# Optimization experiments

Measured on AMD Instinct MI355X. Metric: run time of the kernel, lower is better.

Reference implementation:

```python
import jax, jax.numpy as jnp
import numpy as np

E = 64      # embedding_dim
H = 64      # h_dim
MLP = 1024  # mlp_dim (attention hidden)
PRE1 = 512  # mlp_pre_pool hidden
BNK = 1024  # bottleneck_dim
S = 256     # num scenes (equal-size groups replacing seq_start_end)
P = 16      # pedestrians per scene
B = S * P   # total batch of pedestrians
T = 8       # obs_len for vx/vy (only last row used)
EPS = 1e-5  # BatchNorm eps


def _bn(x, g, b, m, v):
    # eval-mode BatchNorm1d over the last (feature) axis
    return (x - m) * jax.lax.rsqrt(v + EPS) * g + b


def setup_inputs() -> dict:
    key = jax.random.key(0)
    ks = jax.random.split(key, 24)
    def n(k, shape, s=1.0):
        return jax.random.normal(k, shape, jnp.float32) * s
    return {
        "h_states": n(ks[0], (1, B, H)),
        "end_pos": n(ks[1], (B, 2)),
        "vx": n(ks[2], (T, B)),
        "vy": n(ks[3], (T, B)),
        "W_sp": n(ks[4], (2, E), 0.05), "b_sp": jnp.zeros((E,), jnp.float32),
        "W_vel": n(ks[5], (2, E), 0.05), "b_vel": jnp.zeros((E,), jnp.float32),
        "Wa1": n(ks[6], (2 * E, MLP), 0.05), "ba1": jnp.zeros((MLP,), jnp.float32),
        "ga1": jnp.ones((MLP,), jnp.float32), "bta1": jnp.zeros((MLP,), jnp.float32),
        "ma1": n(ks[7], (MLP,), 0.1), "va1": jax.random.uniform(ks[8], (MLP,), jnp.float32) + 0.5,
        "Wa2": n(ks[9], (MLP, 1), 0.05), "ba2": jnp.zeros((1,), jnp.float32),
        "ga2": jnp.ones((1,), jnp.float32), "bta2": jnp.zeros((1,), jnp.float32),
        "ma2": n(ks[10], (1,), 0.1), "va2": jax.random.uniform(ks[11], (1,), jnp.float32) + 0.5,
        "Wp1": n(ks[12], (E + H, PRE1), 0.05), "bp1": jnp.zeros((PRE1,), jnp.float32),
        "gp1": jnp.ones((PRE1,), jnp.float32), "btp1": jnp.zeros((PRE1,), jnp.float32),
        "mp1": n(ks[13], (PRE1,), 0.1), "vp1": jax.random.uniform(ks[14], (PRE1,), jnp.float32) + 0.5,
        "Wp2": n(ks[15], (PRE1, BNK), 0.05), "bp2": jnp.zeros((BNK,), jnp.float32),
        "gp2": jnp.ones((BNK,), jnp.float32), "btp2": jnp.zeros((BNK,), jnp.float32),
        "mp2": n(ks[16], (BNK,), 0.1), "vp2": jax.random.uniform(ks[17], (BNK,), jnp.float32) + 0.5,
        "num_scenes": S, "num_ped": P,
    }


def _forward(h_states, end_pos, vx, vy, W_sp, b_sp, W_vel, b_vel,
             Wa1, ba1, ga1, bta1, ma1, va1, Wa2, ba2, ga2, bta2, ma2, va2,
             Wp1, bp1, gp1, btp1, mp1, vp1, Wp2, bp2, gp2, btp2, mp2, vp2,
             num_scenes, num_ped):
    Sn, Pn = num_scenes, num_ped
    h = h_states.reshape(-1, H).reshape(Sn, Pn, H)          # per-scene hidden
    pos = end_pos.reshape(Sn, Pn, 2)
    # rel[s,i,j] = pos[s,j] - pos[s,i]  (repeat vs repeat_interleave in torch)
    rel = pos[:, None, :, :] - pos[:, :, None, :]
    rel_emb = rel @ W_sp + b_sp                              # [S,P,P,E]
    vel = jnp.stack([vx[-1], vy[-1]], axis=-1).reshape(Sn, Pn, 2)
    vel_emb = vel @ W_vel + b_vel                            # [S,P,E], indexed by row i
    vel_emb = jnp.broadcast_to(vel_emb[:, :, None, :], (Sn, Pn, Pn, E))
    att_in = jnp.concatenate([rel_emb, vel_emb], axis=-1)    # [S,P,P,2E]
    a = jax.nn.relu(_bn(att_in @ Wa1 + ba1, ga1, bta1, ma1, va1))
    scores = jax.nn.relu(_bn(a @ Wa2 + ba2, ga2, bta2, ma2, va2))  # [S,P,P,1]
    # torch.softmax(scores, dim=1) on an (N,1) tensor: softmax over the size-1
    # feature axis -> identically 1.0. Reproduced faithfully here.
    w = jax.nn.softmax(scores, axis=-1)
    h_rep = jnp.broadcast_to(h[:, None, :, :], (Sn, Pn, Pn, H))   # h[s,j] per (i,j)
    x = jnp.concatenate([rel_emb, h_rep], axis=-1) * (0.05 * w)   # [S,P,P,E+H]
    y = jax.nn.relu(_bn(x @ Wp1 + bp1, gp1, btp1, mp1, vp1))
    y = jax.nn.relu(_bn(y @ Wp2 + bp2, gp2, btp2, mp2, vp2))      # [S,P,P,BNK]
    pool = jnp.max(y, axis=2)                                     # max over neighbors j
    return pool.reshape(Sn * Pn, BNK)


def reference(h_states, end_pos, vx, vy, W_sp, b_sp, W_vel, b_vel,
              Wa1, ba1, ga1, bta1, ma1, va1, Wa2, ba2, ga2, bta2, ma2, va2,
              Wp1, bp1, gp1, btp1, mp1, vp1, Wp2, bp2, gp2, btp2, mp2, vp2,
              num_scenes, num_ped):
    return _forward(h_states, end_pos, vx, vy, W_sp, b_sp, W_vel, b_vel,
                    Wa1, ba1, ga1, bta1, ma1, va1, Wa2, ba2, ga2, bta2, ma2, va2,
                    Wp1, bp1, gp1, btp1, mp1, vp1, Wp2, bp2, gp2, btp2, mp2, vp2,
                    num_scenes, num_ped)
```

## Files before the change

kernel.cpp:

```cpp
#include <hip/hip_runtime.h>
#include <hip/hip_bf16.h>
#include <stdint.h>


typedef __bf16 bf16x8 __attribute__((ext_vector_type(8)));
typedef __bf16 bf16x2 __attribute__((ext_vector_type(2)));
typedef float  f32x4  __attribute__((ext_vector_type(4)));
typedef float  f32x2  __attribute__((ext_vector_type(2)));
typedef float  f32x16 __attribute__((ext_vector_type(16)));

#define BP2_OFF 0u
#define BP1_OFF 1048576u
#define MX_OFF  1114112u
#define MY_OFF  1116160u
#define CB_OFF  1118208u
#define SH_OFF  1120256u
#define A2_OFF  1122304u
#define C2_OFF  1126400u

#define Y1_LDS  0
#define HH_LDS  131072
#define LDS_SZ  147456

__device__ __forceinline__ unsigned short f2bf(float f) {
    union { float f; unsigned u; } c; c.f = f;
    unsigned u = c.u;
    return (unsigned short)((u + 0x7fffu + ((u >> 16) & 1u)) >> 16);
}
__device__ __forceinline__ float bfbits2f(unsigned hi) {
    union { unsigned u; float f; } c; c.u = hi; return c.f;
}
__device__ __forceinline__ unsigned pk_bf16(float a, float b) {
#if __has_builtin(__builtin_amdgcn_cvt_pk_bf16_f32)
    bf16x2 p = __builtin_amdgcn_cvt_pk_bf16_f32(a, b);
    union { bf16x2 v; unsigned u; } c; c.v = p; return c.u;
#else
    return (unsigned)f2bf(a) | ((unsigned)f2bf(b) << 16);
#endif
}
__device__ __forceinline__ int y1off(int r, int c16) {
    return r * 1024 + ((c16 ^ (r & 7)) << 4);
}

__global__ __launch_bounds__(256) void prep_pack_kernel(
    const float* __restrict__ Wsp,  const float* __restrict__ bsp,
    const float* __restrict__ Wp1,  const float* __restrict__ bp1,
    const float* __restrict__ gp1,  const float* __restrict__ btp1,
    const float* __restrict__ mp1,  const float* __restrict__ vp1,
    const float* __restrict__ Wp2,  const float* __restrict__ bp2,
    const float* __restrict__ gp2,  const float* __restrict__ btp2,
    const float* __restrict__ mp2,  const float* __restrict__ vp2,
    unsigned char* __restrict__ ws)
{
    __shared__ float tile[32 * 65];
    const int blk = blockIdx.x, t = threadIdx.x;

    if (blk < 272) {
        const float* src; int ncols, kb, ng;
        if (blk < 256) { kb = blk >> 4; ng = blk & 15; src = Wp2; ncols = 1024; }
        else { int b2 = blk - 256; kb = b2 >> 3; ng = b2 & 7; src = Wp1 + 64 * 512; ncols = 512; }
        const int k0 = kb * 32, n0 = ng * 64;
        #pragma unroll
        for (int it = 0; it < 2; ++it) {
            int c = t + it * 256;
            int r = c >> 4, c4 = c & 15;
            float4 v = *(const float4*)(src + (k0 + r) * ncols + n0 + c4 * 4);
            tile[r * 65 + c4 * 4 + 0] = v.x;
            tile[r * 65 + c4 * 4 + 1] = v.y;
            tile[r * 65 + c4 * 4 + 2] = v.z;
            tile[r * 65 + c4 * 4 + 3] = v.w;
        }
        __syncthreads();
        if (blk < 256) {
            const int l = t & 63, ch = (t >> 6) & 1, kh = t >> 7;
            const int nl = ch * 32 + (l & 31);
            const int kl = kh * 16 + ((l >> 5) & 1) * 8;
            uint4 o;
            o.x = pk_bf16(tile[(kl + 0) * 65 + nl], tile[(kl + 1) * 65 + nl]);
            o.y = pk_bf16(tile[(kl + 2) * 65 + nl], tile[(kl + 3) * 65 + nl]);
            o.z = pk_bf16(tile[(kl + 4) * 65 + nl], tile[(kl + 5) * 65 + nl]);
            o.w = pk_bf16(tile[(kl + 6) * 65 + nl], tile[(kl + 7) * 65 + nl]);
            const int kstep = kb * 2 + kh, ct = ng * 2 + ch;
            ((uint4*)(ws + BP2_OFF))[(kstep * 32 + ct) * 64 + l] = o;
        } else {
            int ntl = t >> 6, l = t & 63;
            int nl = ntl * 16 + (l & 15), kl = (l >> 4) * 8;
            uint4 o;
            o.x = pk_bf16(tile[(kl + 0) * 65 + nl], tile[(kl + 1) * 65 + nl]);
            o.y = pk_bf16(tile[(kl + 2) * 65 + nl], tile[(kl + 3) * 65 + nl]);
            o.z = pk_bf16(tile[(kl + 4) * 65 + nl], tile[(kl + 5) * 65 + nl]);
            o.w = pk_bf16(tile[(kl + 6) * 65 + nl], tile[(kl + 7) * 65 + nl]);
            ((uint4*)(ws + BP1_OFF))[((ng * 4 + ntl) * 2 + kb) * 64 + l] = o;
        }
    } else if (blk < 274) {
        int k = (blk - 272) * 256 + t;
        float a1 = gp1[k] * rsqrtf(vp1[k] + 1e-5f);
        float mx = 0.f, my = 0.f, cb = 0.f;
        for (int e = 0; e < 64; ++e) {
            float wv = Wp1[e * 512 + k];
            mx = fmaf(Wsp[e],      wv, mx);
            my = fmaf(Wsp[64 + e], wv, my);
            cb = fmaf(bsp[e],      wv, cb);
        }
        ((float*)(ws + MX_OFF))[k] = 0.05f * a1 * mx;
        ((float*)(ws + MY_OFF))[k] = 0.05f * a1 * my;
        ((float*)(ws + CB_OFF))[k] = 0.05f * a1 * cb + (bp1[k] - mp1[k]) * a1 + btp1[k];
        ((float*)(ws + SH_OFF))[k] = 0.05f * a1;
    } else {
        int n = (blk - 274) * 256 + t;
        float a = gp2[n] * rsqrtf(vp2[n] + 1e-5f);
        ((float*)(ws + A2_OFF))[n] = a;
        ((float*)(ws + C2_OFF))[n] = btp2[n] + (bp2[n] - mp2[n]) * a;
    }
}

__global__ __launch_bounds__(512, 2) void mm2_kernel(
    const float* __restrict__ hst,
    const float* __restrict__ epos,
    const unsigned char* __restrict__ ws,
    float* __restrict__ out)
{
    __shared__ __align__(16) unsigned char smem[LDS_SZ];

    const int s   = blockIdx.x >> 1;
    const int ih  = blockIdx.x & 1;
    const int tid = threadIdx.x;
    const int w    = tid >> 6;
    const int l    = tid & 63;
    const int quad = l >> 4;
    const int jl   = l & 15;

    {
        union { unsigned u[4]; bf16x8 v; } afh[2];
        #pragma unroll
        for (int kb = 0; kb < 2; ++kb) {
            const float4* hp = (const float4*)(hst + (s * 16 + jl) * 64 + kb * 32 + quad * 8);
            float4 v0 = hp[0], v1 = hp[1];
            afh[kb].u[0] = pk_bf16(v0.x, v0.y);
            afh[kb].u[1] = pk_bf16(v0.z, v0.w);
            afh[kb].u[2] = pk_bf16(v1.x, v1.y);
            afh[kb].u[3] = pk_bf16(v1.z, v1.w);
        }
        const f32x4 fz = {0.f, 0.f, 0.f, 0.f};
        f32x4 acch[4] = {fz, fz, fz, fz};
        #pragma unroll
        for (int kb = 0; kb < 2; ++kb) {
            #pragma unroll
            for (int ct = 0; ct < 4; ++ct) {
                bf16x8 bfr = *(const bf16x8*)(ws + BP1_OFF + ((((w * 4 + ct) * 2 + kb) * 64 + l) << 4));
                acch[ct] = __builtin_amdgcn_mfma_f32_16x16x32_bf16(afh[kb].v, bfr, acch[ct], 0, 0, 0);
            }
        }
        const float* SHg = (const float*)(ws + SH_OFF);
        const float* CBg = (const float*)(ws + CB_OFF);
        #pragma unroll
        for (int ct = 0; ct < 4; ++ct) {
            int col = (w * 4 + ct) * 16 + jl;
            float sh = SHg[col], cb = CBg[col];
            #pragma unroll
            for (int reg = 0; reg < 4; ++reg) {
                int j = quad * 4 + reg;
                float hv = fmaf(acch[ct][reg], sh, cb);
                *(unsigned short*)(smem + HH_LDS + j * 1024 + col * 2) = f2bf(hv);
            }
        }
    }
    __syncthreads();

    {
        const int i2 = tid >> 8;
        const int j  = (tid >> 4) & 15;
        const int kc = tid & 15;
        float rx[4], ry[4];
        float pjx = epos[s * 32 + j * 2], pjy = epos[s * 32 + j * 2 + 1];
        #pragma unroll
        for (int ii = 0; ii < 4; ++ii) {
            int ig_ = ih * 8 + i2 * 4 + ii;
            rx[ii] = pjx - epos[s * 32 + ig_ * 2];
            ry[ii] = pjy - epos[s * 32 + ig_ * 2 + 1];
        }
        const f32x2 zero2 = {0.f, 0.f};
        #pragma unroll
        for (int kk = 0; kk < 4; ++kk) {
            int k = kc * 32 + kk * 8;
            uint4 hh8 = *(const uint4*)(smem + HH_LDS + j * 1024 + k * 2);
            f32x4 mx0 = *(const f32x4*)(ws + MX_OFF + k * 4);
            f32x4 mx1 = *(const f32x4*)(ws + MX_OFF + k * 4 + 16);
            f32x4 my0 = *(const f32x4*)(ws + MY_OFF + k * 4);
            f32x4 my1 = *(const f32x4*)(ws + MY_OFF + k * 4 + 16);
            f32x2 mxp[4] = { {mx0[0],mx0[1]}, {mx0[2],mx0[3]}, {mx1[0],mx1[1]}, {mx1[2],mx1[3]} };
            f32x2 myp[4] = { {my0[0],my0[1]}, {my0[2],my0[3]}, {my1[0],my1[1]}, {my1[2],my1[3]} };
            f32x2 hhp[4];
            hhp[0][0] = bfbits2f(hh8.x << 16); hhp[0][1] = bfbits2f(hh8.x & 0xffff0000u);
            hhp[1][0] = bfbits2f(hh8.y << 16); hhp[1][1] = bfbits2f(hh8.y & 0xffff0000u);
            hhp[2][0] = bfbits2f(hh8.z << 16); hhp[2][1] = bfbits2f(hh8.z & 0xffff0000u);
            hhp[3][0] = bfbits2f(hh8.w << 16); hhp[3][1] = bfbits2f(hh8.w & 0xffff0000u);
            #pragma unroll
            for (int ii = 0; ii < 4; ++ii) {
                f32x2 rx2 = { rx[ii], rx[ii] };
                f32x2 ry2 = { ry[ii], ry[ii] };
                uint4 o;
                unsigned uu[4];
                #pragma unroll
                for (int p = 0; p < 4; ++p) {
                    f32x2 tt = __builtin_elementwise_fma(ry2, myp[p], hhp[p]);
                    tt = __builtin_elementwise_fma(rx2, mxp[p], tt);
                    tt = __builtin_elementwise_max(tt, zero2);
                    uu[p] = pk_bf16(tt[0], tt[1]);
                }
                o.x = uu[0]; o.y = uu[1]; o.z = uu[2]; o.w = uu[3];
                int r = (i2 * 4 + ii) * 16 + j;
                *(uint4*)(smem + Y1_LDS + y1off(r, kc * 4 + kk)) = o;
            }
        }
    }
    __syncthreads();

    {
        const int lane31 = l & 31;
        const int hi = l >> 5;
        const int sr = lane31 & 7;
        const float* A2 = (const float*)(ws + A2_OFF);
        const float* C2 = (const float*)(ws + C2_OFF);

        int av[4];
        #pragma unroll
        for (int rt = 0; rt < 4; ++rt)
            av[rt] = Y1_LDS + (rt * 32 + lane31) * 1024 + ((hi ^ sr) << 4);

        const f32x16 fz16 = {0.f,0.f,0.f,0.f,0.f,0.f,0.f,0.f,
                             0.f,0.f,0.f,0.f,0.f,0.f,0.f,0.f};

        #pragma unroll 1
        for (int chunk = 0; chunk < 2; ++chunk) {
            const int ctbase = w * 4 + chunk * 2;
            const unsigned char* bp = ws + BP2_OFF + (ctbase << 10) + (l << 4);

            f32x16 acc[4][2];
            #pragma unroll
            for (int rt = 0; rt < 4; ++rt) { acc[rt][0] = fz16; acc[rt][1] = fz16; }

            bf16x8 a0[4], a1[4];
            bf16x8 br[4][2];

            auto ldA = [&](bf16x8* dst, int add, int xorv) {
                #pragma unroll
                for (int rt = 0; rt < 4; ++rt)
                    dst[rt] = *(const bf16x8*)(smem + ((av[rt] + add) ^ xorv));
            };
            auto ldB = [&](bf16x8* slot, const unsigned char* base, int off) {
                slot[0] = *(const bf16x8*)(base + off);
                slot[1] = *(const bf16x8*)(base + off + 1024);
            };
            auto mfma8 = [&](const bf16x8* a, const bf16x8* b) {
                __builtin_amdgcn_s_setprio(1);
                #pragma unroll
                for (int c = 0; c < 2; ++c)
                    #pragma unroll
                    for (int rt = 0; rt < 4; ++rt)
                        acc[rt][c] = __builtin_amdgcn_mfma_f32_32x32x16_bf16(
                            a[rt], b[c], acc[rt][c], 0, 0, 0);
                __builtin_amdgcn_s_setprio(0);
            };

            ldB(br[0], bp, 0);
            ldB(br[1], bp, 32768);
            ldB(br[2], bp, 65536);
            ldA(a0, 0, 0);

            #pragma unroll 1
            for (int kq = 0; kq < 7; ++kq) {
                const unsigned char* bq = bp + kq * 131072;
                const int ka = kq * 128;
                ldB(br[3], bq, 98304);
                ldA(a1, ka, 32);
                mfma8(a0, br[0]);
                ldB(br[0], bq, 131072);
                ldA(a0, ka, 64);
                mfma8(a1, br[1]);
                ldB(br[1], bq, 163840);
                ldA(a1, ka, 96);
                mfma8(a0, br[2]);
                ldB(br[2], bq, 196608);
                ldA(a0, ka + 128, 0);
                mfma8(a1, br[3]);
            }
            {
                const unsigned char* bq = bp + 7 * 131072;
                const int ka = 7 * 128;
                ldB(br[3], bq, 98304);
                ldA(a1, ka, 32);
                mfma8(a0, br[0]);
                ldA(a0, ka, 64);
                mfma8(a1, br[1]);
                ldA(a1, ka, 96);
                mfma8(a0, br[2]);
                mfma8(a1, br[3]);
            }

            #pragma unroll
            for (int c = 0; c < 2; ++c) {
                const int col = (ctbase + c) * 32 + lane31;
                const float a2 = A2[col], c2v = C2[col];
                #pragma unroll
                for (int rt = 0; rt < 4; ++rt) {
                    float mv[2];
                    #pragma unroll
                    for (int hg = 0; hg < 2; ++hg) {
                        float v0 = fmaxf(fmaf(acc[rt][c][hg * 8 + 0], a2, c2v), 0.f);
                        float v1 = fmaxf(fmaf(acc[rt][c][hg * 8 + 1], a2, c2v), 0.f);
                        float v2 = fmaxf(fmaf(acc[rt][c][hg * 8 + 2], a2, c2v), 0.f);
                        float v3 = fmaxf(fmaf(acc[rt][c][hg * 8 + 3], a2, c2v), 0.f);
                        float v4 = fmaxf(fmaf(acc[rt][c][hg * 8 + 4], a2, c2v), 0.f);
                        float v5 = fmaxf(fmaf(acc[rt][c][hg * 8 + 5], a2, c2v), 0.f);
                        float v6 = fmaxf(fmaf(acc[rt][c][hg * 8 + 6], a2, c2v), 0.f);
                        float v7 = fmaxf(fmaf(acc[rt][c][hg * 8 + 7], a2, c2v), 0.f);
                        float m = fmaxf(fmaxf(fmaxf(v0, v1), fmaxf(v2, v3)),
                                        fmaxf(fmaxf(v4, v5), fmaxf(v6, v7)));
                        mv[hg] = fmaxf(m, __shfl_xor(m, 32, 64));
                    }
                    const int iloc = rt * 2 + hi;
                    const float vout = hi ? mv[1] : mv[0];
                    const int orow = s * 16 + ih * 8 + iloc;
                    __builtin_nontemporal_store(vout, &out[orow * 1024 + col]);
                }
            }
        }
    }
}

extern "C" void kernel_launch(void* const* d_in, const int* in_sizes, int n_in,
                              void* d_out, int out_size, void* d_ws, size_t ws_size,
                              hipStream_t stream) {
    const float* hst  = (const float*)d_in[0];
    const float* epos = (const float*)d_in[1];
    const float* Wsp  = (const float*)d_in[4];
    const float* bsp  = (const float*)d_in[5];
    const float* Wp1  = (const float*)d_in[20];
    const float* bp1  = (const float*)d_in[21];
    const float* gp1  = (const float*)d_in[22];
    const float* btp1 = (const float*)d_in[23];
    const float* mp1  = (const float*)d_in[24];
    const float* vp1  = (const float*)d_in[25];
    const float* Wp2  = (const float*)d_in[26];
    const float* bp2  = (const float*)d_in[27];
    const float* gp2  = (const float*)d_in[28];
    const float* btp2 = (const float*)d_in[29];
    const float* mp2  = (const float*)d_in[30];
    const float* vp2  = (const float*)d_in[31];
    unsigned char* ws = (unsigned char*)d_ws;
    float* out = (float*)d_out;

    prep_pack_kernel<<<278, 256, 0, stream>>>(Wsp, bsp, Wp1, bp1, gp1, btp1, mp1, vp1,
                                              Wp2, bp2, gp2, btp2, mp2, vp2, ws);
    mm2_kernel<<<512, 512, 0, stream>>>(hst, epos, ws, out);
}
```

Baseline: 192.1 us.

## Software-pipeline across column chunks with explicit waitcnts and split prep reduction

The two column-chunk GEMM loops in mm2_kernel are flattened so that B loads for the second chunk are issued before the first chunk's epilogue, and explicit s_waitcnt with sched barriers replace compiler-inserted waits, keeping more loads in flight. B loads become nontemporal, setprio calls are dropped, and the BN scale/shift loads are hoisted into registers. The prep kernel's per-k reduction over the embedding dimension is split across four thread groups with an LDS reduction over more blocks, and the y1 LDS write pattern is changed to interleave columns. Hand-written waitcnt counts are fragile and could cause races or stalls if they miscount outstanding operations.

```diff
diff --git a/kernel.cpp b/kernel.cpp
--- a/kernel.cpp
+++ b/kernel.cpp
@@ -21,6 +21,9 @@
 #define Y1_LDS  0
 #define HH_LDS  131072
 #define LDS_SZ  147456
+
+#define WAITCNT(S) do { asm volatile("s_waitcnt " S ::: "memory"); \
+                        __builtin_amdgcn_sched_barrier(0); } while (0)
 
 __device__ __forceinline__ unsigned short f2bf(float f) {
     union { float f; unsigned u; } c; c.f = f;
@@ -53,6 +56,7 @@
     unsigned char* __restrict__ ws)
 {
     __shared__ float tile[32 * 65];
+    __shared__ float part[3][4][64];
     const int blk = blockIdx.x, t = threadIdx.x;
 
     if (blk < 272) {
@@ -92,22 +96,33 @@
             o.w = pk_bf16(tile[(kl + 6) * 65 + nl], tile[(kl + 7) * 65 + nl]);
             ((uint4*)(ws + BP1_OFF))[((ng * 4 + ntl) * 2 + kb) * 64 + l] = o;
         }
-    } else if (blk < 274) {
-        int k = (blk - 272) * 256 + t;
-        float a1 = gp1[k] * rsqrtf(vp1[k] + 1e-5f);
+    } else if (blk < 280) {
+        const int kk = t & 63, eq = t >> 6;
+        const int k = (blk - 272) * 64 + kk;
         float mx = 0.f, my = 0.f, cb = 0.f;
-        for (int e = 0; e < 64; ++e) {
+        #pragma unroll
+        for (int e2 = 0; e2 < 16; ++e2) {
+            int e = eq * 16 + e2;
             float wv = Wp1[e * 512 + k];
             mx = fmaf(Wsp[e],      wv, mx);
             my = fmaf(Wsp[64 + e], wv, my);
             cb = fmaf(bsp[e],      wv, cb);
         }
-        ((float*)(ws + MX_OFF))[k] = 0.05f * a1 * mx;
-        ((float*)(ws + MY_OFF))[k] = 0.05f * a1 * my;
-        ((float*)(ws + CB_OFF))[k] = 0.05f * a1 * cb + (bp1[k] - mp1[k]) * a1 + btp1[k];
-        ((float*)(ws + SH_OFF))[k] = 0.05f * a1;
+        part[0][eq][kk] = mx; part[1][eq][kk] = my; part[2][eq][kk] = cb;
+        __syncthreads();
+        if (t < 64) {
+            const int k2 = (blk - 272) * 64 + t;
+            float mxs = part[0][0][t] + part[0][1][t] + part[0][2][t] + part[0][3][t];
+            float mys = part[1][0][t] + part[1][1][t] + part[1][2][t] + part[1][3][t];
+            float cbs = part[2][0][t] + part[2][1][t] + part[2][2][t] + part[2][3][t];
+            float a1 = gp1[k2] * rsqrtf(vp1[k2] + 1e-5f);
+            ((float*)(ws + MX_OFF))[k2] = 0.05f * a1 * mxs;
+            ((float*)(ws + MY_OFF))[k2] = 0.05f * a1 * mys;
+            ((float*)(ws + CB_OFF))[k2] = 0.05f * a1 * cbs + (bp1[k2] - mp1[k2]) * a1 + btp1[k2];
+            ((float*)(ws + SH_OFF))[k2] = 0.05f * a1;
+        }
     } else {
-        int n = (blk - 274) * 256 + t;
+        int n = (blk - 280) * 256 + t;
         float a = gp2[n] * rsqrtf(vp2[n] + 1e-5f);
         ((float*)(ws + A2_OFF))[n] = a;
         ((float*)(ws + C2_OFF))[n] = btp2[n] + (bp2[n] - mp2[n]) * a;
@@ -182,7 +197,8 @@
         const f32x2 zero2 = {0.f, 0.f};
         #pragma unroll
         for (int kk = 0; kk < 4; ++kk) {
-            int k = kc * 32 + kk * 8;
+            int c16 = kk * 16 + kc;
+            int k = c16 * 8;
             uint4 hh8 = *(const uint4*)(smem + HH_LDS + j * 1024 + k * 2);
             f32x4 mx0 = *(const f32x4*)(ws + MX_OFF + k * 4);
             f32x4 mx1 = *(const f32x4*)(ws + MX_OFF + k * 4 + 16);
@@ -210,7 +226,7 @@
                 }
                 o.x = uu[0]; o.y = uu[1]; o.z = uu[2]; o.w = uu[3];
                 int r = (i2 * 4 + ii) * 16 + j;
-                *(uint4*)(smem + Y1_LDS + y1off(r, kc * 4 + kk)) = o;
+                *(uint4*)(smem + Y1_LDS + y1off(r, c16)) = o;
             }
         }
     }
@@ -231,90 +247,49 @@
         const f32x16 fz16 = {0.f,0.f,0.f,0.f,0.f,0.f,0.f,0.f,
                              0.f,0.f,0.f,0.f,0.f,0.f,0.f,0.f};
 
-        #pragma unroll 1
-        for (int chunk = 0; chunk < 2; ++chunk) {
-            const int ctbase = w * 4 + chunk * 2;
-            const unsigned char* bp = ws + BP2_OFF + (ctbase << 10) + (l << 4);
-
-            f32x16 acc[4][2];
-            #pragma unroll
-            for (int rt = 0; rt < 4; ++rt) { acc[rt][0] = fz16; acc[rt][1] = fz16; }
-
-            bf16x8 a0[4], a1[4];
-            bf16x8 br[4][2];
-
-            auto ldA = [&](bf16x8* dst, int add, int xorv) {
+        const int ctb0 = w * 4;
+        const unsigned char* bp = ws + BP2_OFF + (ctb0 << 10) + (l << 4);
+
+        f32x16 acc[4][2];
+        bf16x8 a0[4], a1[4];
+        bf16x8 br[4][2];
+        float a2v[2], c2v[2];
+
+        auto ldA = [&](bf16x8* dst, int add, int xorv) {
+            #pragma unroll
+            for (int rt = 0; rt < 4; ++rt)
+                dst[rt] = *(const bf16x8*)(smem + ((av[rt] + add) ^ xorv));
+        };
+        auto ldB = [&](bf16x8* slot, const unsigned char* p) {
+            slot[0] = __builtin_nontemporal_load((const bf16x8*)p);
+            slot[1] = __builtin_nontemporal_load((const bf16x8*)(p + 1024));
+        };
+        auto mfma8 = [&](const bf16x8* a, const bf16x8* b) {
+            #pragma unroll
+            for (int c = 0; c < 2; ++c)
                 #pragma unroll
                 for (int rt = 0; rt < 4; ++rt)
-                    dst[rt] = *(const bf16x8*)(smem + ((av[rt] + add) ^ xorv));
-            };
-            auto ldB = [&](bf16x8* slot, const unsigned char* base, int off) {
-                slot[0] = *(const bf16x8*)(base + off);
-                slot[1] = *(const bf16x8*)(base + off + 1024);
-            };
-            auto mfma8 = [&](const bf16x8* a, const bf16x8* b) {
-                __builtin_amdgcn_s_setprio(1);
-                #pragma unroll
-                for (int c = 0; c < 2; ++c)
-                    #pragma unroll
-                    for (int rt = 0; rt < 4; ++rt)
-                        acc[rt][c] = __builtin_amdgcn_mfma_f32_32x32x16_bf16(
-                            a[rt], b[c], acc[rt][c], 0, 0, 0);
-                __builtin_amdgcn_s_setprio(0);
-            };
-
-            ldB(br[0], bp, 0);
-            ldB(br[1], bp, 32768);
-            ldB(br[2], bp, 65536);
-            ldA(a0, 0, 0);
-
-            #pragma unroll 1
-            for (int kq = 0; kq < 7; ++kq) {
-                const unsigned char* bq = bp + kq * 131072;
-                const int ka = kq * 128;
-                ldB(br[3], bq, 98304);
-                ldA(a1, ka, 32);
-                mfma8(a0, br[0]);
-                ldB(br[0], bq, 131072);
-                ldA(a0, ka, 64);
-                mfma8(a1, br[1]);
-                ldB(br[1], bq, 163840);
-                ldA(a1, ka, 96);
-                mfma8(a0, br[2]);
-                ldB(br[2], bq, 196608);
-                ldA(a0, ka + 128, 0);
-                mfma8(a1, br[3]);
-            }
-            {
-                const unsigned char* bq = bp + 7 * 131072;
-                const int ka = 7 * 128;
-                ldB(br[3], bq, 98304);
-                ldA(a1, ka, 32);
-                mfma8(a0, br[0]);
-                ldA(a0, ka, 64);
-                mfma8(a1, br[1]);
-                ldA(a1, ka, 96);
-                mfma8(a0, br[2]);
-                mfma8(a1, br[3]);
-            }
-
+                    acc[rt][c] = __builtin_amdgcn_mfma_f32_32x32x16_bf16(
+                        a[rt], b[c], acc[rt][c], 0, 0, 0);
+        };
+        auto epilogue = [&](int ctb) {
             #pragma unroll
             for (int c = 0; c < 2; ++c) {
-                const int col = (ctbase + c) * 32 + lane31;
-                const float a2 = A2[col], c2v = C2[col];
+                const int col = (ctb + c) * 32 + lane31;
+                const float a2 = a2v[c], c2 = c2v[c];
                 #pragma unroll
                 for (int rt = 0; rt < 4; ++rt) {
                     float mv[2];
                     #pragma unroll
                     for (int hg = 0; hg < 2; ++hg) {
-                        float v0 = fmaxf(fmaf(acc[rt][c][hg * 8 + 0], a2, c2v), 0.f);
-                        float v1 = fmaxf(fmaf(acc[rt][c][hg * 8 + 1], a2, c2v), 0.f);
-                        float v2 = fmaxf(fmaf(acc[rt][c][hg * 8 + 2], a2, c2v), 0.f);
-                        float v3 = fmaxf(fmaf(acc[rt][c][hg * 8 + 3], a2, c2v), 0.f);
-                        float v4 = fmaxf(fmaf(acc[rt][c][hg * 8 + 4], a2, c2v), 0.f);
-                        float v5 = fmaxf(fmaf(acc[rt][c][hg * 8 + 5], a2, c2v), 0.f);
-                        float v6 = fmaxf(fmaf(acc[rt][c][hg * 8 + 6], a2, c2v), 0.f);
-                        float v7 = fmaxf(fmaf(acc[rt][c][hg * 8 + 7], a2, c2v), 0.f);
+                        float v0 = fmaxf(fmaf(acc[rt][c][hg * 8 + 0], a2, c2), 0.f);
+                        float v1 = fmaxf(fmaf(acc[rt][c][hg * 8 + 1], a2, c2), 0.f);
+                        float v2 = fmaxf(fmaf(acc[rt][c][hg * 8 + 2], a2, c2), 0.f);
+                        float v3 = fmaxf(fmaf(acc[rt][c][hg * 8 + 3], a2, c2), 0.f);
+                        float v4 = fmaxf(fmaf(acc[rt][c][hg * 8 + 4], a2, c2), 0.f);
+                        float v5 = fmaxf(fmaf(acc[rt][c][hg * 8 + 5], a2, c2), 0.f);
+                        float v6 = fmaxf(fmaf(acc[rt][c][hg * 8 + 6], a2, c2), 0.f);
+                        float v7 = fmaxf(fmaf(acc[rt][c][hg * 8 + 7], a2, c2), 0.f);
                         float m = fmaxf(fmaxf(fmaxf(v0, v1), fmaxf(v2, v3)),
                                         fmaxf(fmaxf(v4, v5), fmaxf(v6, v7)));
                         mv[hg] = fmaxf(m, __shfl_xor(m, 32, 64));
@@ -325,7 +300,87 @@
                     __builtin_nontemporal_store(vout, &out[orow * 1024 + col]);
                 }
             }
-        }
+        };
+
+        a2v[0] = A2[ctb0 * 32 + lane31];        a2v[1] = A2[(ctb0 + 1) * 32 + lane31];
+        c2v[0] = C2[ctb0 * 32 + lane31];        c2v[1] = C2[(ctb0 + 1) * 32 + lane31];
+        #pragma unroll
+        for (int rt = 0; rt < 4; ++rt) { acc[rt][0] = fz16; acc[rt][1] = fz16; }
+        ldB(br[0], bp);
+        ldB(br[1], bp + 32768);
+        ldB(br[2], bp + 65536);
+        ldA(a0, 0, 0);
+
+        #pragma unroll 1
+        for (int kq = 0; kq < 7; ++kq) {
+            const unsigned char* bq = bp + kq * 131072;
+            const int ka = kq * 128;
+            ldB(br[3], bq + 98304);  ldA(a1, ka, 32);
+            WAITCNT("vmcnt(6) lgkmcnt(4)");  mfma8(a0, br[0]);
+            ldB(br[0], bq + 131072); ldA(a0, ka, 64);
+            WAITCNT("vmcnt(6) lgkmcnt(4)");  mfma8(a1, br[1]);
+            ldB(br[1], bq + 163840); ldA(a1, ka, 96);
+            WAITCNT("vmcnt(6) lgkmcnt(4)");  mfma8(a0, br[2]);
+            ldB(br[2], bq + 196608); ldA(a0, ka + 128, 0);
+            WAITCNT("vmcnt(6) lgkmcnt(4)");  mfma8(a1, br[3]);
+        }
+        {
+            const unsigned char* bq = bp + 7 * 131072;
+            const unsigned char* b1 = bp + 2048;
+            const int ka = 7 * 128;
+            ldB(br[3], bq + 98304);  ldA(a1, ka, 32);
+            WAITCNT("vmcnt(6) lgkmcnt(4)");  mfma8(a0, br[0]);
+            ldB(br[0], b1);          ldA(a0, ka, 64);
+            WAITCNT("vmcnt(6) lgkmcnt(4)");  mfma8(a1, br[1]);
+            ldB(br[1], b1 + 32768);  ldA(a1, ka, 96);
+            WAITCNT("vmcnt(6) lgkmcnt(4)");  mfma8(a0, br[2]);
+            ldB(br[2], b1 + 65536);  ldA(a0, 0, 0);
+            WAITCNT("vmcnt(6) lgkmcnt(4)");  mfma8(a1, br[3]);
+        }
+        __builtin_amdgcn_sched_barrier(0);
+        epilogue(ctb0);
+        a2v[0] = A2[(ctb0 + 2) * 32 + lane31];  a2v[1] = A2[(ctb0 + 3) * 32 + lane31];
+        c2v[0] = C2[(ctb0 + 2) * 32 + lane31];  c2v[1] = C2[(ctb0 + 3) * 32 + lane31];
+        #pragma unroll
+        for (int rt = 0; rt < 4; ++rt) { acc[rt][0] = fz16; acc[rt][1] = fz16; }
+        __builtin_amdgcn_sched_barrier(0);
+        {
+            const unsigned char* bq = bp + 2048;
+            ldB(br[3], bq + 98304);  ldA(a1, 0, 32);
+            WAITCNT("vmcnt(18) lgkmcnt(4)"); mfma8(a0, br[0]);
+            ldB(br[0], bq + 131072); ldA(a0, 0, 64);
+            WAITCNT("vmcnt(18) lgkmcnt(4)"); mfma8(a1, br[1]);
+            ldB(br[1], bq + 163840); ldA(a1, 0, 96);
+            WAITCNT("vmcnt(18) lgkmcnt(4)"); mfma8(a0, br[2]);
+            ldB(br[2], bq + 196608); ldA(a0, 128, 0);
+            WAITCNT("vmcnt(6) lgkmcnt(4)");  mfma8(a1, br[3]);
+        }
+        #pragma unroll 1
+        for (int kq = 1; kq < 7; ++kq) {
+            const unsigned char* bq = bp + 2048 + kq * 131072;
+            const int ka = kq * 128;
+            ldB(br[3], bq + 98304);  ldA(a1, ka, 32);
+            WAITCNT("vmcnt(6) lgkmcnt(4)");  mfma8(a0, br[0]);
+            ldB(br[0], bq + 131072); ldA(a0, ka, 64);
+            WAITCNT("vmcnt(6) lgkmcnt(4)");  mfma8(a1, br[1]);
+            ldB(br[1], bq + 163840); ldA(a1, ka, 96);
+            WAITCNT("vmcnt(6) lgkmcnt(4)");  mfma8(a0, br[2]);
+            ldB(br[2], bq + 196608); ldA(a0, ka + 128, 0);
+            WAITCNT("vmcnt(6) lgkmcnt(4)");  mfma8(a1, br[3]);
+        }
+        {
+            const unsigned char* bq = bp + 2048 + 7 * 131072;
+            const int ka = 7 * 128;
+            ldB(br[3], bq + 98304);  ldA(a1, ka, 32);
+            WAITCNT("vmcnt(6) lgkmcnt(4)");  mfma8(a0, br[0]);
+            ldA(a0, ka, 64);
+            WAITCNT("vmcnt(4) lgkmcnt(4)");  mfma8(a1, br[1]);
+            ldA(a1, ka, 96);
+            WAITCNT("vmcnt(2) lgkmcnt(4)");  mfma8(a0, br[2]);
+            WAITCNT("vmcnt(0) lgkmcnt(0)");  mfma8(a1, br[3]);
+        }
+        __builtin_amdgcn_sched_barrier(0);
+        epilogue(ctb0 + 2);
     }
 }
 
@@ -351,7 +406,7 @@
     unsigned char* ws = (unsigned char*)d_ws;
     float* out = (float*)d_out;
 
-    prep_pack_kernel<<<278, 256, 0, stream>>>(Wsp, bsp, Wp1, bp1, gp1, btp1, mp1, vp1,
+    prep_pack_kernel<<<284, 256, 0, stream>>>(Wsp, bsp, Wp1, bp1, gp1, btp1, mp1, vp1,
                                               Wp2, bp2, gp2, btp2, mp2, vp2, ws);
     mm2_kernel<<<512, 512, 0, stream>>>(hst, epos, ws, out);
 }
```

After: 188.3 us. 1.02x faster.
